# Optimization experiments

Hardware: AMD Instinct MI355X
Metric: run time of the kernel (lower is better)

## Reference

```python
import jax, jax.numpy as jnp
import numpy as np

R = 256        # reservoir_size
M = 256        # samples
S = 512        # steps
D = 2          # n_features (dims)
B = 16         # bits_per_feature
LUT_LEN = 18   # 2**18 LUT entries per node; >= max possible state index
OUT = 32       # output_size


def _first_primes(n):
    lim = 2000  # p_256 = 1619 < 2000
    is_p = np.ones(lim, dtype=bool)
    is_p[:2] = False
    for i in range(2, int(lim ** 0.5) + 1):
        if is_p[i]:
            is_p[i * i::i] = False
    return np.nonzero(is_p)[0][:n].astype(np.int32)


def setup_inputs() -> dict:
    key = jax.random.key(0)
    k = jax.random.split(key, 6)
    x = jax.random.randint(k[0], (M, S, D, B), 0, 2).astype(bool)
    lut = jax.random.randint(k[1], (R, 2 ** LUT_LEN), 0, 2).astype(jnp.int32)
    init_res = jax.random.randint(k[2], (R,), 0, 2).astype(bool)
    W = jax.random.randint(k[3], (R, R), 0, 2).astype(bool)
    primes = jnp.asarray(_first_primes(R))  # first R primes, like primes[:reservoir_size]
    input_nodes = jax.random.permutation(k[4], R)[: D * B]  # randperm(R)[:b*d]
    readout_w = jax.random.normal(k[5], (OUT, R), jnp.float32) * (1.0 / np.sqrt(R))
    readout_b = jnp.zeros((OUT,), jnp.float32)
    return dict(x=x, lut=lut, init_res=init_res, W=W, primes=primes,
                input_nodes=input_nodes, readout_w=readout_w, readout_b=readout_b)


def reference(x, lut, init_res, W, primes, input_nodes, readout_w, readout_b):
    m, s, d, b = x.shape
    r = init_res.shape[0]
    xs = x.reshape(m, s, d * b).transpose(1, 0, 2)  # [s, m, nb] time-major for scan
    Wi = W.astype(jnp.int32)                        # [R, R]
    node_idx = jnp.arange(r)                        # [R]

    def step(res, xt):
        # 1. write encoded input bits into the reservoir (scatter)
        res = res.at[:, input_nodes].set(xt)                    # [m, R] bool
        # 2. state_idx[n] = sum_k res[k] * primes[k] * W[n, k]  (primes-weighted masked sum)
        v = res.astype(jnp.int32) * primes                      # [m, R]
        state_idx = v @ Wi.T                                    # [m, R] int32
        # 3. per-node LUT gather -> next boolean state
        res = lut[node_idx[None, :], state_idx].astype(bool)    # [m, R]
        return res, None

    res0 = jnp.broadcast_to(init_res, (m, r))  # every sample starts from initial_reservoir
    res_final, _ = jax.lax.scan(step, res0, xs)
    # readout on final reservoir state
    return res_final.astype(jnp.float32) @ readout_w.T + readout_b  # [m, OUT]
```

## Files before the change

### kernel.cpp

```cpp
#include <hip/hip_runtime.h>
#include <hip/hip_fp16.h>

#define RES 256
#define MS 256
#define ST 512
#define NB 32
#define LUTLEN 262144
#define LUTW 8192
#define NOUT 32
#define NBLK 256

typedef __attribute__((ext_vector_type(8))) _Float16 half8;
typedef __attribute__((ext_vector_type(4))) float f32x4;

__device__ __forceinline__ void publish_barrier() {
    asm volatile("s_waitcnt lgkmcnt(0)" ::: "memory");
    __builtin_amdgcn_s_barrier();
}

__global__ __launch_bounds__(256) void lut_offsets_kernel(const int* __restrict__ W,
                                                          const int* __restrict__ primes,
                                                          int* __restrict__ off) {
    __shared__ int s[RES];
    const int n = threadIdx.x;
    int maxsum = 0;
    for (int k = 0; k < RES; ++k)
        maxsum += (W[n * RES + k] != 0) ? primes[k] : 0;
    int nw = (maxsum >> 5) + 1;
    s[n] = nw;
    __syncthreads();
    for (int d = 1; d < RES; d <<= 1) {
        int v = (n >= d) ? s[n - d] : 0;
        __syncthreads();
        s[n] += v;
        __syncthreads();
    }
    off[n] = s[n] - nw;
    if (n == RES - 1) off[RES] = s[n];
}

__global__ __launch_bounds__(512) void pack_lut2_kernel(const int* __restrict__ lut,
                                                        const int* __restrict__ off,
                                                        unsigned* __restrict__ lutp) {
    const int n = blockIdx.x;
    const int o = off[n];
    const int nw = off[n + 1] - o;
    const int* src = lut + (size_t)n * LUTLEN;
    for (int w = threadIdx.x; w < nw; w += blockDim.x) {
        const int4* p = (const int4*)(src + (size_t)w * 32);
        unsigned word = 0u;
#pragma unroll
        for (int c = 0; c < 8; ++c) {
            const int4 v = p[c];
            word |= (v.x != 0 ? 1u : 0u) << (4 * c + 0);
            word |= (v.y != 0 ? 1u : 0u) << (4 * c + 1);
            word |= (v.z != 0 ? 1u : 0u) << (4 * c + 2);
            word |= (v.w != 0 ? 1u : 0u) << (4 * c + 3);
        }
        lutp[o + w] = word;
    }
}

__global__ __launch_bounds__(256) void pack_x_kernel(const int* __restrict__ x,
                                                     unsigned* __restrict__ xp) {
    const int total = MS * ST;
    int w = blockIdx.x * blockDim.x + threadIdx.x;
    const int stride = gridDim.x * blockDim.x;
    for (; w < total; w += stride) {
        const int4* p = (const int4*)(x + (size_t)w * 32);
        unsigned word = 0u;
#pragma unroll
        for (int c = 0; c < 8; ++c) {
            const int4 v = p[c];
            word |= (v.x != 0 ? 1u : 0u) << (4 * c + 0);
            word |= (v.y != 0 ? 1u : 0u) << (4 * c + 1);
            word |= (v.z != 0 ? 1u : 0u) << (4 * c + 2);
            word |= (v.w != 0 ? 1u : 0u) << (4 * c + 3);
        }
        const int m = w >> 9;
        const int t = w & (ST - 1);
        xp[t * MS + m] = word;
    }
}

template<bool LP, bool XP>
__global__ __launch_bounds__(512) void reservoir_kernel(
    const int* __restrict__ xraw,
    const unsigned* __restrict__ xp,
    const int* __restrict__ lutraw,
    const unsigned* __restrict__ lutp,
    const int* __restrict__ off,
    const int* __restrict__ init_res,
    const int* __restrict__ W,
    const int* __restrict__ primes,
    const int* __restrict__ input_nodes,
    const float* __restrict__ rw,
    const float* __restrict__ rb,
    float* __restrict__ out)
{
    __shared__ __align__(16) _Float16 vArow[2][264];
    __shared__ unsigned xw_lds[ST];

    const int tid = threadIdx.x;
    const int lane = tid & 63;
    const int wid = tid >> 6;
    const int g = lane >> 4;
    const int r = lane & 15;
    const int m0 = blockIdx.x;

    const int nn = wid * 32 + (lane & 31);
    const bool own = (lane < 32);

    const int n0 = wid * 32 + r;
    const int n1 = n0 + 16;

    const _Float16 pz = (_Float16)(float)primes[nn];
    const _Float16 z  = (_Float16)0.0f;

    const unsigned* lpn = LP ? (lutp + off[nn]) : nullptr;
    int jn = -1;
    for (int j = 0; j < NB; ++j)
        if (input_nodes[j] == nn) jn = j;

    half8 B0[8], B1[8];
#pragma unroll
    for (int kc = 0; kc < 8; ++kc) {
        const int kb = kc * 32 + g * 8;
        const int4* w0p = (const int4*)(W + n0 * RES + kb);
        const int4* w1p = (const int4*)(W + n1 * RES + kb);
        const int4 wa = w0p[0], wb = w0p[1], wc = w1p[0], wd = w1p[1];
        half8 b0, b1;
        b0[0] = wa.x != 0 ? (_Float16)1.0f : z;  b0[1] = wa.y != 0 ? (_Float16)1.0f : z;
        b0[2] = wa.z != 0 ? (_Float16)1.0f : z;  b0[3] = wa.w != 0 ? (_Float16)1.0f : z;
        b0[4] = wb.x != 0 ? (_Float16)1.0f : z;  b0[5] = wb.y != 0 ? (_Float16)1.0f : z;
        b0[6] = wb.z != 0 ? (_Float16)1.0f : z;  b0[7] = wb.w != 0 ? (_Float16)1.0f : z;
        b1[0] = wc.x != 0 ? (_Float16)1.0f : z;  b1[1] = wc.y != 0 ? (_Float16)1.0f : z;
        b1[2] = wc.z != 0 ? (_Float16)1.0f : z;  b1[3] = wc.w != 0 ? (_Float16)1.0f : z;
        b1[4] = wd.x != 0 ? (_Float16)1.0f : z;  b1[5] = wd.y != 0 ? (_Float16)1.0f : z;
        b1[6] = wd.z != 0 ? (_Float16)1.0f : z;  b1[7] = wd.w != 0 ? (_Float16)1.0f : z;
        B0[kc] = b0; B1[kc] = b1;
    }

    if (XP) xw_lds[tid] = xp[tid * MS + m0];

    if (own) {
        int b;
        if (XP) {
            const unsigned x0 = xp[m0];
            b = (jn >= 0) ? (int)((x0 >> jn) & 1u) : (init_res[nn] != 0);
        } else {
            b = (jn >= 0) ? (xraw[(m0 * ST) * NB + jn] != 0) : (init_res[nn] != 0);
        }
        vArow[0][nn] = b ? pz : z;
    }
    __syncthreads();

    auto STEP = [&](int cur, int nxt, int t) {
        unsigned xa = 0u;
        if (XP) xa = xw_lds[(t + 1) & (ST - 1)];
        half8 A[8];
#pragma unroll
        for (int kc = 0; kc < 8; ++kc)
            A[kc] = *(const half8*)&vArow[cur][kc * 32 + g * 8];
        f32x4 a0 = {0.f,0.f,0.f,0.f}, a1 = {0.f,0.f,0.f,0.f};
        f32x4 a2 = {0.f,0.f,0.f,0.f}, a3 = {0.f,0.f,0.f,0.f};
        f32x4 b0 = {0.f,0.f,0.f,0.f}, b1 = {0.f,0.f,0.f,0.f};
        f32x4 b2 = {0.f,0.f,0.f,0.f}, b3 = {0.f,0.f,0.f,0.f};
        a0 = __builtin_amdgcn_mfma_f32_16x16x32_f16(A[0], B0[0], a0, 0, 0, 0);
        b0 = __builtin_amdgcn_mfma_f32_16x16x32_f16(A[0], B1[0], b0, 0, 0, 0);
        a1 = __builtin_amdgcn_mfma_f32_16x16x32_f16(A[1], B0[1], a1, 0, 0, 0);
        b1 = __builtin_amdgcn_mfma_f32_16x16x32_f16(A[1], B1[1], b1, 0, 0, 0);
        a2 = __builtin_amdgcn_mfma_f32_16x16x32_f16(A[2], B0[2], a2, 0, 0, 0);
        b2 = __builtin_amdgcn_mfma_f32_16x16x32_f16(A[2], B1[2], b2, 0, 0, 0);
        a3 = __builtin_amdgcn_mfma_f32_16x16x32_f16(A[3], B0[3], a3, 0, 0, 0);
        b3 = __builtin_amdgcn_mfma_f32_16x16x32_f16(A[3], B1[3], b3, 0, 0, 0);
        a0 = __builtin_amdgcn_mfma_f32_16x16x32_f16(A[4], B0[4], a0, 0, 0, 0);
        b0 = __builtin_amdgcn_mfma_f32_16x16x32_f16(A[4], B1[4], b0, 0, 0, 0);
        a1 = __builtin_amdgcn_mfma_f32_16x16x32_f16(A[5], B0[5], a1, 0, 0, 0);
        b1 = __builtin_amdgcn_mfma_f32_16x16x32_f16(A[5], B1[5], b1, 0, 0, 0);
        a2 = __builtin_amdgcn_mfma_f32_16x16x32_f16(A[6], B0[6], a2, 0, 0, 0);
        b2 = __builtin_amdgcn_mfma_f32_16x16x32_f16(A[6], B1[6], b2, 0, 0, 0);
        a3 = __builtin_amdgcn_mfma_f32_16x16x32_f16(A[7], B0[7], a3, 0, 0, 0);
        b3 = __builtin_amdgcn_mfma_f32_16x16x32_f16(A[7], B1[7], b3, 0, 0, 0);

        if (own) {
            const float fa = (a0[0] + a1[0]) + (a2[0] + a3[0]);
            const float fb = (b0[0] + b1[0]) + (b2[0] + b3[0]);
            const float f = (g == 0) ? fa : fb;
            const unsigned i = (unsigned)f;
            int b;
            if (LP) {
                const unsigned w = lpn[i >> 5];
                b = (int)((w >> (i & 31u)) & 1u);
            } else {
                b = (lutraw[(size_t)nn * LUTLEN + i] != 0);
            }
            if (t != ST - 1 && jn >= 0) {
                b = XP ? (int)((xa >> jn) & 1u)
                       : (xraw[(m0 * ST + t + 1) * NB + jn] != 0);
            }
            vArow[nxt][nn] = b ? pz : z;
        }
        publish_barrier();
    };

#pragma unroll 1
    for (int tt = 0; tt < ST; tt += 2) {
        STEP(0, 1, tt);
        STEP(1, 0, tt + 1);
    }

    if (tid < NOUT) {
        const int o = tid;
        float acc = rb[o];
        for (int n = 0; n < RES; ++n) {
            if (vArow[0][n] != z) acc += rw[o * RES + n];
        }
        out[m0 * NOUT + o] = acc;
    }
}

extern "C" void kernel_launch(void* const* d_in, const int* in_sizes, int n_in,
                              void* d_out, int out_size, void* d_ws, size_t ws_size,
                              hipStream_t stream) {
    const int* x           = (const int*)d_in[0];
    const int* lut         = (const int*)d_in[1];
    const int* init_res    = (const int*)d_in[2];
    const int* W           = (const int*)d_in[3];
    const int* primes      = (const int*)d_in[4];
    const int* input_nodes = (const int*)d_in[5];
    const float* rw        = (const float*)d_in[6];
    const float* rb        = (const float*)d_in[7];
    float* out = (float*)d_out;

    const size_t lutp_bytes = (size_t)RES * LUTW * sizeof(unsigned);
    const size_t xp_bytes   = (size_t)ST * MS * sizeof(unsigned);
    const size_t off_bytes  = (RES + 1) * sizeof(int);

    unsigned* lutp = nullptr;
    unsigned* xp = nullptr;
    int* off = nullptr;
    bool use_lp = false, use_xp = false;
    unsigned char* ws = (unsigned char*)d_ws;
    if (ws_size >= lutp_bytes + xp_bytes + 256 + off_bytes) {
        lutp = (unsigned*)ws;
        xp = (unsigned*)(ws + lutp_bytes);
        off = (int*)(ws + lutp_bytes + xp_bytes);
        use_lp = use_xp = true;
    } else if (ws_size >= xp_bytes) {
        xp = (unsigned*)ws;
        use_xp = true;
    }

    if (use_lp) {
        hipLaunchKernelGGL(lut_offsets_kernel, dim3(1), dim3(256), 0, stream, W, primes, off);
        hipLaunchKernelGGL(pack_lut2_kernel, dim3(RES), dim3(512), 0, stream, lut, off, lutp);
    }
    if (use_xp) hipLaunchKernelGGL(pack_x_kernel, dim3(512), dim3(256), 0, stream, x, xp);

    if (use_lp)
        hipLaunchKernelGGL((reservoir_kernel<true, true>), dim3(NBLK), dim3(512), 0, stream,
                           x, xp, lut, lutp, off, init_res, W, primes, input_nodes, rw, rb, out);
    else if (use_xp)
        hipLaunchKernelGGL((reservoir_kernel<false, true>), dim3(NBLK), dim3(512), 0, stream,
                           x, xp, lut, lutp, off, init_res, W, primes, input_nodes, rw, rb, out);
    else
        hipLaunchKernelGGL((reservoir_kernel<false, false>), dim3(NBLK), dim3(512), 0, stream,
                           x, xp, lut, lutp, off, init_res, W, primes, input_nodes, rw, rb, out);
}
```

Before: 373.5 us.

## Halve reservoir block to 4 waves, each wave computing 64 nodes with 4 MFMA tiles

The reservoir kernel drops from 8 waves per block to 4. Each wave now owns 64 nodes instead of 32, so it keeps 4 column tiles of W in registers and runs 32 MFMAs per step, and all 64 lanes do a LUT lookup instead of half of them. This makes each wave do more work per barrier and cuts the per-step barrier cost, which now spans fewer waves. In exchange each wave carries a longer serial MFMA chain and higher register pressure (B[4][8] half8), so per-step latency could grow.

Result: slower. 428.8 us (+14.8%).

```diff
diff --git a/kernel.cpp b/kernel.cpp
--- a/kernel.cpp
+++ b/kernel.cpp
@@ -84,7 +84,7 @@
 }
 
 template<bool LP, bool XP>
-__global__ __launch_bounds__(512) void reservoir_kernel(
+__global__ __launch_bounds__(256, 1) void reservoir_kernel(
     const int* __restrict__ xraw,
     const unsigned* __restrict__ xp,
     const int* __restrict__ lutraw,
@@ -108,11 +108,7 @@
     const int r = lane & 15;
     const int m0 = blockIdx.x;
 
-    const int nn = wid * 32 + (lane & 31);
-    const bool own = (lane < 32);
-
-    const int n0 = wid * 32 + r;
-    const int n1 = n0 + 16;
+    const int nn = wid * 64 + lane;
 
     const _Float16 pz = (_Float16)(float)primes[nn];
     const _Float16 z  = (_Float16)0.0f;
@@ -122,28 +118,30 @@
     for (int j = 0; j < NB; ++j)
         if (input_nodes[j] == nn) jn = j;
 
-    half8 B0[8], B1[8];
-#pragma unroll
-    for (int kc = 0; kc < 8; ++kc) {
-        const int kb = kc * 32 + g * 8;
-        const int4* w0p = (const int4*)(W + n0 * RES + kb);
-        const int4* w1p = (const int4*)(W + n1 * RES + kb);
-        const int4 wa = w0p[0], wb = w0p[1], wc = w1p[0], wd = w1p[1];
-        half8 b0, b1;
-        b0[0] = wa.x != 0 ? (_Float16)1.0f : z;  b0[1] = wa.y != 0 ? (_Float16)1.0f : z;
-        b0[2] = wa.z != 0 ? (_Float16)1.0f : z;  b0[3] = wa.w != 0 ? (_Float16)1.0f : z;
-        b0[4] = wb.x != 0 ? (_Float16)1.0f : z;  b0[5] = wb.y != 0 ? (_Float16)1.0f : z;
-        b0[6] = wb.z != 0 ? (_Float16)1.0f : z;  b0[7] = wb.w != 0 ? (_Float16)1.0f : z;
-        b1[0] = wc.x != 0 ? (_Float16)1.0f : z;  b1[1] = wc.y != 0 ? (_Float16)1.0f : z;
-        b1[2] = wc.z != 0 ? (_Float16)1.0f : z;  b1[3] = wc.w != 0 ? (_Float16)1.0f : z;
-        b1[4] = wd.x != 0 ? (_Float16)1.0f : z;  b1[5] = wd.y != 0 ? (_Float16)1.0f : z;
-        b1[6] = wd.z != 0 ? (_Float16)1.0f : z;  b1[7] = wd.w != 0 ? (_Float16)1.0f : z;
-        B0[kc] = b0; B1[kc] = b1;
-    }
-
-    if (XP) xw_lds[tid] = xp[tid * MS + m0];
-
-    if (own) {
+    half8 B[4][8];
+#pragma unroll
+    for (int tau = 0; tau < 4; ++tau) {
+        const int nc = wid * 64 + tau * 16 + r;
+#pragma unroll
+        for (int kc = 0; kc < 8; ++kc) {
+            const int kb = kc * 32 + g * 8;
+            const int4* wp = (const int4*)(W + nc * RES + kb);
+            const int4 wa = wp[0], wb = wp[1];
+            half8 b;
+            b[0] = wa.x != 0 ? (_Float16)1.0f : z;  b[1] = wa.y != 0 ? (_Float16)1.0f : z;
+            b[2] = wa.z != 0 ? (_Float16)1.0f : z;  b[3] = wa.w != 0 ? (_Float16)1.0f : z;
+            b[4] = wb.x != 0 ? (_Float16)1.0f : z;  b[5] = wb.y != 0 ? (_Float16)1.0f : z;
+            b[6] = wb.z != 0 ? (_Float16)1.0f : z;  b[7] = wb.w != 0 ? (_Float16)1.0f : z;
+            B[tau][kc] = b;
+        }
+    }
+
+    if (XP) {
+        xw_lds[tid] = xp[tid * MS + m0];
+        xw_lds[tid + 256] = xp[(tid + 256) * MS + m0];
+    }
+
+    {
         int b;
         if (XP) {
             const unsigned x0 = xp[m0];
@@ -162,45 +160,35 @@
 #pragma unroll
         for (int kc = 0; kc < 8; ++kc)
             A[kc] = *(const half8*)&vArow[cur][kc * 32 + g * 8];
-        f32x4 a0 = {0.f,0.f,0.f,0.f}, a1 = {0.f,0.f,0.f,0.f};
-        f32x4 a2 = {0.f,0.f,0.f,0.f}, a3 = {0.f,0.f,0.f,0.f};
-        f32x4 b0 = {0.f,0.f,0.f,0.f}, b1 = {0.f,0.f,0.f,0.f};
-        f32x4 b2 = {0.f,0.f,0.f,0.f}, b3 = {0.f,0.f,0.f,0.f};
-        a0 = __builtin_amdgcn_mfma_f32_16x16x32_f16(A[0], B0[0], a0, 0, 0, 0);
-        b0 = __builtin_amdgcn_mfma_f32_16x16x32_f16(A[0], B1[0], b0, 0, 0, 0);
-        a1 = __builtin_amdgcn_mfma_f32_16x16x32_f16(A[1], B0[1], a1, 0, 0, 0);
-        b1 = __builtin_amdgcn_mfma_f32_16x16x32_f16(A[1], B1[1], b1, 0, 0, 0);
-        a2 = __builtin_amdgcn_mfma_f32_16x16x32_f16(A[2], B0[2], a2, 0, 0, 0);
-        b2 = __builtin_amdgcn_mfma_f32_16x16x32_f16(A[2], B1[2], b2, 0, 0, 0);
-        a3 = __builtin_amdgcn_mfma_f32_16x16x32_f16(A[3], B0[3], a3, 0, 0, 0);
-        b3 = __builtin_amdgcn_mfma_f32_16x16x32_f16(A[3], B1[3], b3, 0, 0, 0);
-        a0 = __builtin_amdgcn_mfma_f32_16x16x32_f16(A[4], B0[4], a0, 0, 0, 0);
-        b0 = __builtin_amdgcn_mfma_f32_16x16x32_f16(A[4], B1[4], b0, 0, 0, 0);
-        a1 = __builtin_amdgcn_mfma_f32_16x16x32_f16(A[5], B0[5], a1, 0, 0, 0);
-        b1 = __builtin_amdgcn_mfma_f32_16x16x32_f16(A[5], B1[5], b1, 0, 0, 0);
-        a2 = __builtin_amdgcn_mfma_f32_16x16x32_f16(A[6], B0[6], a2, 0, 0, 0);
-        b2 = __builtin_amdgcn_mfma_f32_16x16x32_f16(A[6], B1[6], b2, 0, 0, 0);
-        a3 = __builtin_amdgcn_mfma_f32_16x16x32_f16(A[7], B0[7], a3, 0, 0, 0);
-        b3 = __builtin_amdgcn_mfma_f32_16x16x32_f16(A[7], B1[7], b3, 0, 0, 0);
-
-        if (own) {
-            const float fa = (a0[0] + a1[0]) + (a2[0] + a3[0]);
-            const float fb = (b0[0] + b1[0]) + (b2[0] + b3[0]);
-            const float f = (g == 0) ? fa : fb;
-            const unsigned i = (unsigned)f;
-            int b;
-            if (LP) {
-                const unsigned w = lpn[i >> 5];
-                b = (int)((w >> (i & 31u)) & 1u);
-            } else {
-                b = (lutraw[(size_t)nn * LUTLEN + i] != 0);
+        f32x4 ca[4], cb[4];
+#pragma unroll
+        for (int tau = 0; tau < 4; ++tau) { ca[tau] = {0.f,0.f,0.f,0.f}; cb[tau] = {0.f,0.f,0.f,0.f}; }
+#pragma unroll
+        for (int kc = 0; kc < 8; kc += 2) {
+#pragma unroll
+            for (int tau = 0; tau < 4; ++tau) {
+                ca[tau] = __builtin_amdgcn_mfma_f32_16x16x32_f16(A[kc],   B[tau][kc],   ca[tau], 0, 0, 0);
+                cb[tau] = __builtin_amdgcn_mfma_f32_16x16x32_f16(A[kc+1], B[tau][kc+1], cb[tau], 0, 0, 0);
             }
-            if (t != ST - 1 && jn >= 0) {
-                b = XP ? (int)((xa >> jn) & 1u)
-                       : (xraw[(m0 * ST + t + 1) * NB + jn] != 0);
-            }
-            vArow[nxt][nn] = b ? pz : z;
-        }
+        }
+        float f0 = ca[0][0] + cb[0][0];
+        float f1 = ca[1][0] + cb[1][0];
+        float f2 = ca[2][0] + cb[2][0];
+        float f3 = ca[3][0] + cb[3][0];
+        float f = (g == 0) ? f0 : (g == 1) ? f1 : (g == 2) ? f2 : f3;
+        const unsigned i = (unsigned)f;
+        int b;
+        if (LP) {
+            const unsigned w = lpn[i >> 5];
+            b = (int)((w >> (i & 31u)) & 1u);
+        } else {
+            b = (lutraw[(size_t)nn * LUTLEN + i] != 0);
+        }
+        if (t != ST - 1 && jn >= 0) {
+            b = XP ? (int)((xa >> jn) & 1u)
+                   : (xraw[(m0 * ST + t + 1) * NB + jn] != 0);
+        }
+        vArow[nxt][nn] = b ? pz : z;
         publish_barrier();
     };
 
@@ -259,12 +247,12 @@
     if (use_xp) hipLaunchKernelGGL(pack_x_kernel, dim3(512), dim3(256), 0, stream, x, xp);
 
     if (use_lp)
-        hipLaunchKernelGGL((reservoir_kernel<true, true>), dim3(NBLK), dim3(512), 0, stream,
+        hipLaunchKernelGGL((reservoir_kernel<true, true>), dim3(NBLK), dim3(256), 0, stream,
                            x, xp, lut, lutp, off, init_res, W, primes, input_nodes, rw, rb, out);
     else if (use_xp)
-        hipLaunchKernelGGL((reservoir_kernel<false, true>), dim3(NBLK), dim3(512), 0, stream,
+        hipLaunchKernelGGL((reservoir_kernel<false, true>), dim3(NBLK), dim3(256), 0, stream,
                            x, xp, lut, lutp, off, init_res, W, primes, input_nodes, rw, rb, out);
     else
-        hipLaunchKernelGGL((reservoir_kernel<false, false>), dim3(NBLK), dim3(512), 0, stream,
+        hipLaunchKernelGGL((reservoir_kernel<false, false>), dim3(NBLK), dim3(256), 0, stream,
                            x, xp, lut, lutp, off, init_res, W, primes, input_nodes, rw, rb, out);
 }
```
